# Kernel optimization log

Hardware: AMD Instinct MI355X
Metric: run time of the kernel (lower is better)

The kernel has to match this reference:

```python
import jax, jax.numpy as jnp
import numpy as np

N = 65536          # query points (rays * samples per chunk)
C = 2048           # num_codes in code cloud
K = 16             # knn neighbors
CD = 64            # code_dim
IN_XYZ = 63        # positional-encoded xyz channels
IN_DIR = 27        # positional-encoded dir channels
W = 128            # decoder width (D=4, skips=[2])
DIST_SCALE = 2.0


def setup_inputs() -> dict:
    key = jax.random.key(0)
    ks = jax.random.split(key, 16)

    def glorot(k, shape):
        return jax.random.normal(k, shape, jnp.float32) / np.float32(np.sqrt(shape[0]))

    in_x = CD + IN_XYZ  # decoder in_channels_xyz = 127
    inp = {
        "indices": jnp.zeros((1,), jnp.int32),
        "query_points": jax.random.uniform(ks[0], (N, 3), jnp.float32),
        "xyzdir_embedded": jax.random.normal(ks[1], (N, IN_XYZ + IN_DIR), jnp.float32),
        "codes_position": jax.random.uniform(ks[2], (1, C, 3), jnp.float32),
        "codes": jax.random.normal(ks[3], (1, C, CD), jnp.float32) * 0.01,
        # decoder params
        "W0": glorot(ks[4], (in_x, W)), "b0": jnp.zeros((W,), jnp.float32),
        "W1": glorot(ks[5], (W, W)), "b1": jnp.zeros((W,), jnp.float32),
        "W2": glorot(ks[6], (W + in_x, W)), "b2": jnp.zeros((W,), jnp.float32),  # skip layer i=2
        "W3": glorot(ks[7], (W, W)), "b3": jnp.zeros((W,), jnp.float32),
        "Wf": glorot(ks[8], (W, W)), "bf": jnp.zeros((W,), jnp.float32),          # xyz_encoding_final
        "Wd": glorot(ks[9], (W + IN_DIR, W // 2)), "bd": jnp.zeros((W // 2,), jnp.float32),
        "Ws": glorot(ks[10], (W, 1)), "bs": jnp.zeros((1,), jnp.float32),
        "Wr": glorot(ks[11], (W // 2, 3)), "br": jnp.zeros((3,), jnp.float32),
    }
    return inp


def _knn_idx(q, c, k):
    # brute-force L2 knn (faiss replacement); indices only, no grad (torch no_grad)
    q = jax.lax.stop_gradient(q)
    c = jax.lax.stop_gradient(c)
    d2 = (jnp.sum(q * q, -1, keepdims=True)
          - 2.0 * q @ c.T
          + jnp.sum(c * c, -1))  # (N, C)
    _, idx = jax.lax.top_k(-d2, k)  # (N, K) nearest
    return idx


def reference(indices, query_points, xyzdir_embedded, codes_position, codes,
              W0, b0, W1, b1, W2, b2, W3, b3, Wf, bf, Wd, bd, Ws, bs, Wr, br):
    # --- CodeCloud.query ---
    cp = codes_position[indices][0]      # (C, 3)
    cc = codes[indices][0]               # (C, CD)
    idx = _knn_idx(query_points, cp, K)  # (N, K)
    neigh_pos = cp[idx]                  # (N, K, 3)
    sq = jnp.sum((query_points[:, None, :] - neigh_pos) ** 2, -1) + 1e-16  # (N, K)
    w = 1.0 / jnp.sqrt(sq) ** DIST_SCALE
    w = w / jnp.sum(w, -1, keepdims=True)
    neigh_codes = cc[idx]                # (N, K, CD)
    query_codes = jnp.einsum("nk,nkd->nd", w, neigh_codes)  # (N, CD)

    # --- IM_Decoder (D=4, W=128, skips=[2]) ---
    x = jnp.concatenate([query_codes, xyzdir_embedded], -1)  # (N, 127+27)
    in_x = CD + IN_XYZ
    input_xyz, input_dir = x[:, :in_x], x[:, in_x:]
    h = jax.nn.relu(input_xyz @ W0 + b0)
    h = jax.nn.relu(h @ W1 + b1)
    h = jax.nn.relu(jnp.concatenate([input_xyz, h], -1) @ W2 + b2)  # skip at i=2
    h = jax.nn.relu(h @ W3 + b3)
    sigma = h @ Ws + bs                       # (N, 1)
    final = h @ Wf + bf                       # (N, W)
    d = jax.nn.relu(jnp.concatenate([final, input_dir], -1) @ Wd + bd)
    rgb = d @ Wr + br                         # (N, 3)
    return jnp.concatenate([rgb, sigma], -1)  # (N, 4)
```

## Files before the change

kernel.cpp:

```cpp
#include <hip/hip_runtime.h>

#define N_Q   65536
#define N_C   2048
#define KNN_K 16
#define CDIM  64
#define SLCAP 128
#define KINF  0x7FFFFFFF
#define WSZ   108544

typedef _Float16 half_t;
typedef float v4f __attribute__((ext_vector_type(4)));
typedef half_t v8h __attribute__((ext_vector_type(8)));

#define ASTRIDE 136
#define DSTRIDE 40

__device__ __forceinline__ int dppx(int v, int j){
  if (j == 1) return __builtin_amdgcn_mov_dpp(v, 0xB1,  0xF, 0xF, true);
  if (j == 2) return __builtin_amdgcn_mov_dpp(v, 0x4E,  0xF, 0xF, true);
  if (j == 8) return __builtin_amdgcn_mov_dpp(v, 0x128, 0xF, 0xF, true);
  return __shfl_xor(v, j, 64);
}
__device__ __forceinline__ float dppxf(float v, int j){
  return __int_as_float(dppx(__float_as_int(v), j));
}

__device__ __forceinline__ int select16th(int x){
  int P = 0;
#pragma unroll
  for (int b = 30; b >= 0; --b){
    int cand = P | (1 << b);
    unsigned long long m = __ballot(x < cand);
    if ((int)__popcll(m) < 16) P = cand;
  }
  return P;
}

__global__ void wtrans_kernel(const float* W0, const float* W1, const float* W2,
                              const float* W3, const float* Wf, const float* Wd,
                              const int* indices, const float* cpos,
                              half_t* wt, float4* cpos4){
  int idx = blockIdx.x * 256 + threadIdx.x;
  if (idx >= 110592) return;
  if (idx >= WSZ){
    int i = idx - WSZ;
    const float* cp = cpos + (size_t)indices[0] * N_C * 3;
    float x = cp[i*3 + 0], y = cp[i*3 + 1], z = cp[i*3 + 2];
    cpos4[i] = make_float4(x, y, z, fmaf(x, x, fmaf(y, y, fmaf(z, z, 4.0f))));
    return;
  }
  int base, nt, mode;
  const float* src = W1;
  if (idx < 16384){ base = 0; nt = 8; mode = 1; }
  else if (idx < 32768){ base = 16384; nt = 8; mode = 0; src = W1; }
  else if (idx < 65536){ base = 32768; nt = 8; mode = 2; }
  else if (idx < 81920){ base = 65536; nt = 8; mode = 0; src = W3; }
  else if (idx < 98304){ base = 81920; nt = 8; mode = 0; src = Wf; }
  else { base = 98304; nt = 4; mode = 3; }
  int i = idx - base;
  int tile = i >> 9, e = i & 511;
  int lane = e >> 3, j = e & 7;
  int k0idx = tile / nt, tcol = tile - k0idx*nt;
  int n = tcol*16 + (lane & 15);
  int k = k0idx*32 + ((lane >> 4) << 3) + j;
  float val;
  if (mode == 0)      val = src[k*128 + n];
  else if (mode == 1) val = (k < 127) ? W0[k*128 + n] : 0.f;
  else if (mode == 2) val = (k == 127) ? 0.f
                           : ((k < 127) ? W2[k*128 + n] : W2[(k-1)*128 + n]);
  else                val = (k < 155) ? Wd[k*64 + n] : 0.f;
  wt[idx] = (half_t)val;
}

__global__ __launch_bounds__(512, 6) void knn_kernel(const int* indices,
    const float* qpts, const float4* cpos4, const float* codes,
    const float* xyzdir, half_t* Ain, half_t* Din){
  __shared__ float4 lp[N_C];
  __shared__ int    sl[8*SLCAP];
  int tid = threadIdx.x;
  int lane = tid & 63, wave = tid >> 6;
  const float* cc = codes + (size_t)indices[0] * N_C * CDIM;

  for (int c = tid; c < N_C; c += 512) lp[c] = cpos4[c];
  __syncthreads();

  int q = blockIdx.x * 8 + wave;
  float qx = qpts[q*3 + 0];
  float qy = qpts[q*3 + 1];
  float qz = qpts[q*3 + 2];
  float nqx = -2.0f*qx, nqy = -2.0f*qy, nqz = -2.0f*qz;

  int p[32];
#pragma unroll
  for (int j = 0; j < 32; j++){
    int c = j*64 + lane;
    float4 P = lp[c];
    float s = fmaf(P.x, nqx, fmaf(P.y, nqy, fmaf(P.z, nqz, P.w)));
    int pv = (__float_as_int(s) & 0xFFFFF800) | c;
    asm("" : "+v"(pv));
    p[j] = pv;
  }

  int lm = p[0];
#pragma unroll
  for (int j = 1; j < 32; j++) lm = min(lm, p[j]);

  int tau = select16th(lm);

  int* slw = &sl[wave * SLCAP];
  int n = 0;
#pragma unroll
  for (int j = 0; j < 32; j++){
    bool c = (p[j] <= tau);
    unsigned long long m = __ballot(c);
    if (m){
      if (n <= 64){
        if (c){
          int mb = __builtin_amdgcn_mbcnt_hi((unsigned)(m >> 32),
                   __builtin_amdgcn_mbcnt_lo((unsigned)m, 0));
          slw[n + mb] = p[j];
        }
      }
      n += (int)__popcll(m);
    }
  }
  __builtin_amdgcn_wave_barrier();

  int keep;
  if (n >= KNN_K && n <= 64){
    int x = (lane < n) ? slw[lane] : KINF;
    int P2 = select16th(x);
    unsigned long long wmask = __ballot(x <= P2);
    int pos = __builtin_amdgcn_mbcnt_hi((unsigned)(wmask >> 32),
              __builtin_amdgcn_mbcnt_lo((unsigned)wmask, 0));
    if (x <= P2) slw[pos] = x;
    __builtin_amdgcn_wave_barrier();
    keep = (lane < KNN_K) ? slw[lane] : KINF;
  } else {
    keep = KINF;
#pragma unroll 1
    for (int rr = 0; rr < KNN_K; rr++){
      int lmf = p[0];
#pragma unroll
      for (int j = 1; j < 32; j++) lmf = min(lmf, p[j]);
      int gm = lmf;
#pragma unroll
      for (int off2 = 1; off2 < 64; off2 <<= 1)
        gm = min(gm, __shfl_xor(gm, off2, 64));
      if (lane == rr) keep = gm;
#pragma unroll
      for (int j = 0; j < 32; j++) p[j] = (p[j] == gm) ? KINF : p[j];
    }
  }

  int ci = keep & 0x7FF;
  float4 P = lp[ci];
  float dx = qx - P.x, dy = qy - P.y, dz = qz - P.z;
  float d2 = fmaf(dz, dz, fmaf(dy, dy, dx*dx));
  float w = 1.0f / (d2 + 1e-16f);
  float wm = (lane < KNN_K) ? w : 0.0f;
  wm += dppxf(wm, 1);
  wm += dppxf(wm, 2);
  wm += __shfl_xor(wm, 4, 64);
  wm += dppxf(wm, 8);
  float wn = w / wm;

  float acc = 0.f;
#pragma unroll
  for (int i = 0; i < KNN_K; i++){
    int   cb = __shfl(ci, i, 64);
    float wb = __shfl(wn, i, 64);
    acc = fmaf(wb, cc[cb*CDIM + lane], acc);
  }
  size_t arow = (size_t)q * ASTRIDE;
  Ain[arow + lane] = (half_t)acc;

  float xv = (lane < 63) ? xyzdir[(size_t)q*90 + lane] : 0.f;
  Ain[arow + 64 + lane] = (half_t)xv;
  if (lane < 8) Ain[arow + 128 + lane] = (half_t)0.f;
  if (lane < 40){
    float dv = (lane < 27) ? xyzdir[(size_t)q*90 + 63 + lane] : 0.f;
    Din[(size_t)q*DSTRIDE + lane] = (half_t)dv;
  }
}

template<int NCH, int NT>
__device__ inline void mfma_pl(const half_t* act, int astride, int rowbase,
                               const half_t* wlayer, int nt, int ktbase,
                               int tcolbase, v4f acc[2][NT], int lane){
  v8h breg[NCH*NT];
#pragma unroll
  for (int c = 0; c < NCH; c++){
#pragma unroll
    for (int t = 0; t < NT; t++){
      const half_t* bp = wlayer +
          ((size_t)(((ktbase + c)*nt + tcolbase + t) << 9) + (lane << 3));
      breg[c*NT + t] = *(const v8h*)bp;
    }
  }
  int m = lane & 15, quad = lane >> 4;
#pragma unroll
  for (int c = 0; c < NCH; c++){
    v8h a0 = *(const v8h*)&act[(rowbase + m)*astride + c*32 + quad*8];
    v8h a1 = *(const v8h*)&act[(rowbase + 16 + m)*astride + c*32 + quad*8];
#pragma unroll
    for (int t = 0; t < NT; t++){
      acc[0][t] = __builtin_amdgcn_mfma_f32_16x16x32_f16(a0, breg[c*NT + t], acc[0][t], 0, 0, 0);
      acc[1][t] = __builtin_amdgcn_mfma_f32_16x16x32_f16(a1, breg[c*NT + t], acc[1][t], 0, 0, 0);
    }
  }
}

template<int NT>
__device__ inline void epilogue64(v4f acc[2][NT], half_t* outb, int rowbase,
                                  int colbase, const float* bias, bool relu,
                                  int lane){
  int n = lane & 15, quad = lane >> 4;
#pragma unroll
  for (int t = 0; t < NT; t++){
    int col = colbase + t*16 + n;
    float bv = bias[col];
#pragma unroll
    for (int g = 0; g < 2; g++){
#pragma unroll
      for (int r = 0; r < 4; r++){
        float v = acc[g][t][r] + bv;
        if (relu) v = fmaxf(v, 0.f);
        outb[(rowbase + g*16 + quad*4 + r)*ASTRIDE + col] = (half_t)v;
      }
    }
  }
}

__global__ __launch_bounds__(512, 6) void mlp_mfma(
    const half_t* Ain, const half_t* Din, const half_t* wt,
    const float* b0, const float* b1, const float* b2, const float* b3,
    const float* bfb, const float* bdb,
    const float* Wsb, const float* bsb, const float* Wrb, const float* brb,
    float* out){
  __shared__ __align__(16) half_t Abuf[64*ASTRIDE];
  __shared__ __align__(16) half_t Pbuf[64*ASTRIDE];
  __shared__ __align__(16) half_t Qbuf[64*ASTRIDE];

  int tid = threadIdx.x, lane = tid & 63, wave = tid >> 6;
  int qbase = blockIdx.x * 64;

  for (int i = tid; i < 64*17; i += 512){
    int r = i / 17, c8 = i - r*17;
    *(uint4*)&Abuf[r*ASTRIDE + (c8 << 3)] =
        *(const uint4*)&Ain[(size_t)(qbase + r)*ASTRIDE + (c8 << 3)];
  }
  __syncthreads();

  int rowbase  = (wave >> 2) * 32;
  int colq     = wave & 3;
  int colbase  = colq * 32;
  int tcolbase = colq * 2;
  v4f acc[2][2];
  v4f accd[2][1];

  const half_t* wt0 = wt;
  const half_t* wt1 = wt + 16384;
  const half_t* wt2 = wt + 32768;
  const half_t* wt3 = wt + 65536;
  const half_t* wtf = wt + 81920;
  const half_t* wtd = wt + 98304;

#define ZACC22() { for (int g_ = 0; g_ < 2; g_++) for (int t_ = 0; t_ < 2; t_++) \
                   for (int e_ = 0; e_ < 4; e_++) acc[g_][t_][e_] = 0.f; }

  ZACC22();
  mfma_pl<4,2>(Abuf, ASTRIDE, rowbase, wt0, 8, 0, tcolbase, acc, lane);
  epilogue64<2>(acc, Pbuf, rowbase, colbase, b0, true, lane);
  __syncthreads();

  ZACC22();
  mfma_pl<4,2>(Pbuf, ASTRIDE, rowbase, wt1, 8, 0, tcolbase, acc, lane);
  epilogue64<2>(acc, Qbuf, rowbase, colbase, b1, true, lane);
  __syncthreads();

  ZACC22();
  mfma_pl<4,2>(Abuf, ASTRIDE, rowbase, wt2, 8, 0, tcolbase, acc, lane);
  mfma_pl<4,2>(Qbuf, ASTRIDE, rowbase, wt2, 8, 4, tcolbase, acc, lane);
  epilogue64<2>(acc, Pbuf, rowbase, colbase, b2, true, lane);
  __syncthreads();

  ZACC22();
  mfma_pl<4,2>(Pbuf, ASTRIDE, rowbase, wt3, 8, 0, tcolbase, acc, lane);
  epilogue64<2>(acc, Abuf, rowbase, colbase, b3, true, lane);
  __syncthreads();

  ZACC22();
  mfma_pl<4,2>(Abuf, ASTRIDE, rowbase, wtf, 8, 0, tcolbase, acc, lane);
  epilogue64<2>(acc, Pbuf, rowbase, colbase, bfb, false, lane);
  __syncthreads();

#pragma unroll
  for (int g_ = 0; g_ < 2; g_++)
#pragma unroll
    for (int e_ = 0; e_ < 4; e_++) accd[g_][0][e_] = 0.f;
  mfma_pl<4,1>(Pbuf, ASTRIDE, rowbase, wtd, 4, 0, colq, accd, lane);
  mfma_pl<1,1>(Din + (size_t)qbase*DSTRIDE, DSTRIDE, rowbase, wtd, 4, 4, colq,
               accd, lane);
  epilogue64<1>(accd, Qbuf, rowbase, colq * 16, bdb, true, lane);
  __syncthreads();

  {
    int q = tid >> 3, part = tid & 7;
    float s = 0.f;
#pragma unroll
    for (int k = 0; k < 16; k++){
      int kk = part*16 + k;
      s = fmaf((float)Abuf[q*ASTRIDE + kk], Wsb[kk], s);
    }
    s += __shfl_xor(s, 1, 64); s += __shfl_xor(s, 2, 64); s += __shfl_xor(s, 4, 64);

    float r3[3];
#pragma unroll
    for (int c2 = 0; c2 < 3; c2++){
      float rv = 0.f;
#pragma unroll
      for (int k = 0; k < 8; k++){
        int kk = part*8 + k;
        rv = fmaf((float)Qbuf[q*ASTRIDE + kk], Wrb[kk*3 + c2], rv);
      }
      rv += __shfl_xor(rv, 1, 64); rv += __shfl_xor(rv, 2, 64); rv += __shfl_xor(rv, 4, 64);
      r3[c2] = rv;
    }
    if (part == 0){
      size_t ob = ((size_t)(qbase + q)) * 4;
      out[ob + 0] = r3[0] + brb[0];
      out[ob + 1] = r3[1] + brb[1];
      out[ob + 2] = r3[2] + brb[2];
      out[ob + 3] = s + bsb[0];
    }
  }
}

extern "C" void kernel_launch(void* const* d_in, const int* in_sizes, int n_in,
                              void* d_out, int out_size, void* d_ws, size_t ws_size,
                              hipStream_t stream){
  (void)in_sizes; (void)n_in; (void)out_size; (void)ws_size;

  const int*   indices = (const int*)d_in[0];
  const float* qpts    = (const float*)d_in[1];
  const float* xyzdir  = (const float*)d_in[2];
  const float* cpos    = (const float*)d_in[3];
  const float* codes   = (const float*)d_in[4];
  const float* W0 = (const float*)d_in[5];
  const float* b0 = (const float*)d_in[6];
  const float* W1 = (const float*)d_in[7];
  const float* b1 = (const float*)d_in[8];
  const float* W2 = (const float*)d_in[9];
  const float* b2 = (const float*)d_in[10];
  const float* W3 = (const float*)d_in[11];
  const float* b3 = (const float*)d_in[12];
  const float* Wf = (const float*)d_in[13];
  const float* bf = (const float*)d_in[14];
  const float* Wd = (const float*)d_in[15];
  const float* bd = (const float*)d_in[16];
  const float* Ws = (const float*)d_in[17];
  const float* bs = (const float*)d_in[18];
  const float* Wr = (const float*)d_in[19];
  const float* br = (const float*)d_in[20];

  half_t* Ain   = (half_t*)d_ws;
  half_t* Din   = (half_t*)((char*)d_ws + 17825792);
  half_t* wt    = (half_t*)((char*)d_ws + 17825792 + 5242880);
  float4* cpos4 = (float4*)((char*)d_ws + 17825792 + 5242880 + 217088);

  wtrans_kernel<<<(110592 + 255)/256, 256, 0, stream>>>(W0, W1, W2, W3, Wf, Wd,
                                                        indices, cpos, wt, cpos4);
  knn_kernel<<<N_Q/8, 512, 0, stream>>>(indices, qpts, cpos4, codes, xyzdir,
                                        Ain, Din);
  mlp_mfma<<<N_Q/64, 512, 0, stream>>>(Ain, Din, wt,
                                       b0, b1, b2, b3, bf, bd, Ws, bs, Wr, br,
                                       (float*)d_out);
}
```

Before: 203.2 us.

## Use uniform grid candidate lists to prune brute-force KNN search

Adds a grid kernel that bins the 2048 code positions into a 16^3 grid and, for each cell, records candidates lying in a 7^3 neighbourhood. The KNN kernel then scores at most 256 candidates per query instead of all 2048. It checks whether the 16th distance lies within the distance to the neighbourhood boundary and otherwise falls back to an exact streaming brute-force selection. The radix select is also narrowed to fewer bits because the biased distance is known to be at least 4.0. This cuts distance evaluations and register pressure, at the cost of an extra kernel launch, a list lookup and a possible slow fallback path.

```diff
diff --git a/kernel.cpp b/kernel.cpp
--- a/kernel.cpp
+++ b/kernel.cpp
@@ -8,6 +8,10 @@
 #define KINF  0x7FFFFFFF
 #define WSZ   108544
 
+#define GN     16
+#define GCELLS 4096
+#define LCAP   256
+
 typedef _Float16 half_t;
 typedef float v4f __attribute__((ext_vector_type(4)));
 typedef half_t v8h __attribute__((ext_vector_type(8)));
@@ -25,15 +29,42 @@
   return __int_as_float(dppx(__float_as_int(v), j));
 }
 
-__device__ __forceinline__ int select16th(int x){
-  int P = 0;
-#pragma unroll
-  for (int b = 30; b >= 0; --b){
+__device__ __forceinline__ int select16f(int x){
+  int P = 0x40800000;
+#pragma unroll
+  for (int b = 22; b >= 0; --b){
     int cand = P | (1 << b);
     unsigned long long m = __ballot(x < cand);
     if ((int)__popcll(m) < 16) P = cand;
   }
   return P;
+}
+
+__device__ __forceinline__ int knn_fallback(const float4* lp, float nqx,
+                                            float nqy, float nqz, int lane){
+  unsigned used = 0u;
+  int keep = KINF;
+#pragma unroll 1
+  for (int rr = 0; rr < KNN_K; rr++){
+    int best = KINF;
+#pragma unroll 1
+    for (int j = 0; j < 32; j++){
+      int c = j*64 + lane;
+      float4 P = lp[c];
+      float s = fmaf(P.x, nqx, fmaf(P.y, nqy, fmaf(P.z, nqz, P.w)));
+      int pv = (__float_as_int(s) & 0xFFFFF800) | c;
+      pv = ((used >> j) & 1u) ? KINF : pv;
+      best = min(best, pv);
+    }
+    int gm = best;
+#pragma unroll
+    for (int off2 = 1; off2 < 64; off2 <<= 1)
+      gm = min(gm, __shfl_xor(gm, off2, 64));
+    if (lane == rr) keep = gm;
+    int gc = gm & 0x7FF;
+    if ((gc & 63) == lane) used |= (1u << (gc >> 6));
+  }
+  return keep;
 }
 
 __global__ void wtrans_kernel(const float* W0, const float* W1, const float* W2,
@@ -72,9 +103,40 @@
   wt[idx] = (half_t)val;
 }
 
+__global__ __launch_bounds__(512) void grid_kernel(const float4* cpos4,
+    unsigned short* list, int* cnt){
+  int lane = threadIdx.x & 63, wave = threadIdx.x >> 6;
+  int c = blockIdx.x * 8 + wave;
+  int cx = c & 15, cy = (c >> 4) & 15, cz = c >> 8;
+  int lox = min(max(cx - 3, 0), 9);
+  int loy = min(max(cy - 3, 0), 9);
+  int loz = min(max(cz - 3, 0), 9);
+  unsigned short* L = list + (size_t)c * LCAP;
+  int n = 0;
+#pragma unroll 1
+  for (int b = 0; b < 32; b++){
+    int i = b * 64 + lane;
+    float4 P = cpos4[i];
+    int ix = min((int)(P.x * 16.0f), 15);
+    int iy = min((int)(P.y * 16.0f), 15);
+    int iz = min((int)(P.z * 16.0f), 15);
+    bool in = ((unsigned)(ix - lox) < 7u) && ((unsigned)(iy - loy) < 7u) &&
+              ((unsigned)(iz - loz) < 7u);
+    unsigned long long m = __ballot(in);
+    if (m){
+      int mb = __builtin_amdgcn_mbcnt_hi((unsigned)(m >> 32),
+               __builtin_amdgcn_mbcnt_lo((unsigned)m, 0));
+      if (in && (n + mb) < LCAP) L[n + mb] = (unsigned short)i;
+      n += (int)__popcll(m);
+    }
+  }
+  if (lane == 0) cnt[c] = (n <= LCAP) ? n : 0;
+}
+
 __global__ __launch_bounds__(512, 6) void knn_kernel(const int* indices,
-    const float* qpts, const float4* cpos4, const float* codes,
-    const float* xyzdir, half_t* Ain, half_t* Din){
+    const float* qpts, const float4* cpos4, const unsigned short* list,
+    const int* cnt, const float* codes, const float* xyzdir,
+    half_t* Ain, half_t* Din){
   __shared__ float4 lp[N_C];
   __shared__ int    sl[8*SLCAP];
   int tid = threadIdx.x;
@@ -90,35 +152,45 @@
   float qz = qpts[q*3 + 2];
   float nqx = -2.0f*qx, nqy = -2.0f*qy, nqz = -2.0f*qz;
 
-  int p[32];
-#pragma unroll
-  for (int j = 0; j < 32; j++){
-    int c = j*64 + lane;
-    float4 P = lp[c];
+  int cx = min((int)(qx * 16.0f), 15);
+  int cy = min((int)(qy * 16.0f), 15);
+  int cz = min((int)(qz * 16.0f), 15);
+  int cell = cx | (cy << 4) | (cz << 8);
+  int lox = min(max(cx - 3, 0), 9);
+  int loy = min(max(cy - 3, 0), 9);
+  int loz = min(max(cz - 3, 0), 9);
+  int nl = cnt[cell];
+  const unsigned short* L = list + (size_t)cell * LCAP;
+
+  int p[4];
+  int lanemin = KINF;
+#pragma unroll
+  for (int it = 0; it < 4; it++){
+    int j = it*64 + lane;
+    int idx = L[j] & 2047;
+    float4 P = lp[idx];
     float s = fmaf(P.x, nqx, fmaf(P.y, nqy, fmaf(P.z, nqz, P.w)));
-    int pv = (__float_as_int(s) & 0xFFFFF800) | c;
+    int pv = (__float_as_int(s) & 0xFFFFF800) | idx;
+    pv = (j < nl) ? pv : KINF;
     asm("" : "+v"(pv));
-    p[j] = pv;
-  }
-
-  int lm = p[0];
-#pragma unroll
-  for (int j = 1; j < 32; j++) lm = min(lm, p[j]);
-
-  int tau = select16th(lm);
+    p[it] = pv;
+    lanemin = min(lanemin, pv);
+  }
+
+  int tau = select16f(lanemin);
 
   int* slw = &sl[wave * SLCAP];
   int n = 0;
 #pragma unroll
-  for (int j = 0; j < 32; j++){
-    bool c = (p[j] <= tau);
+  for (int it = 0; it < 4; it++){
+    bool c = (p[it] <= tau);
     unsigned long long m = __ballot(c);
     if (m){
       if (n <= 64){
         if (c){
           int mb = __builtin_amdgcn_mbcnt_hi((unsigned)(m >> 32),
                    __builtin_amdgcn_mbcnt_lo((unsigned)m, 0));
-          slw[n + mb] = p[j];
+          slw[n + mb] = p[it];
         }
       }
       n += (int)__popcll(m);
@@ -126,32 +198,30 @@
   }
   __builtin_amdgcn_wave_barrier();
 
-  int keep;
+  int keep = KINF;
+  bool need_fb = true;
   if (n >= KNN_K && n <= 64){
     int x = (lane < n) ? slw[lane] : KINF;
-    int P2 = select16th(x);
+    int P2 = select16f(x);
     unsigned long long wmask = __ballot(x <= P2);
     int pos = __builtin_amdgcn_mbcnt_hi((unsigned)(wmask >> 32),
               __builtin_amdgcn_mbcnt_lo((unsigned)wmask, 0));
     if (x <= P2) slw[pos] = x;
     __builtin_amdgcn_wave_barrier();
     keep = (lane < KNN_K) ? slw[lane] : KINF;
-  } else {
-    keep = KINF;
-#pragma unroll 1
-    for (int rr = 0; rr < KNN_K; rr++){
-      int lmf = p[0];
-#pragma unroll
-      for (int j = 1; j < 32; j++) lmf = min(lmf, p[j]);
-      int gm = lmf;
-#pragma unroll
-      for (int off2 = 1; off2 < 64; off2 <<= 1)
-        gm = min(gm, __shfl_xor(gm, off2, 64));
-      if (lane == rr) keep = gm;
-#pragma unroll
-      for (int j = 0; j < 32; j++) p[j] = (p[j] == gm) ? KINF : p[j];
-    }
-  }
+
+    float d2u = __int_as_float(P2 & 0xFFFFF800) - 4.0f + 0.001f;
+    float lofx = lox * 0.0625f, lofy = loy * 0.0625f, lofz = loz * 0.0625f;
+    float cl = 1e9f;
+    if (lox > 0) cl = fminf(cl, qx - lofx);
+    if (lox < 9) cl = fminf(cl, lofx + 0.4375f - qx);
+    if (loy > 0) cl = fminf(cl, qy - lofy);
+    if (loy < 9) cl = fminf(cl, lofy + 0.4375f - qy);
+    if (loz > 0) cl = fminf(cl, qz - lofz);
+    if (loz < 9) cl = fminf(cl, lofz + 0.4375f - qz);
+    need_fb = !(d2u <= cl * cl);
+  }
+  if (need_fb) keep = knn_fallback(lp, nqx, nqy, nqz, lane);
 
   int ci = keep & 0x7FF;
   float4 P = lp[ci];
@@ -364,15 +434,18 @@
   const float* Wr = (const float*)d_in[19];
   const float* br = (const float*)d_in[20];
 
-  half_t* Ain   = (half_t*)d_ws;
-  half_t* Din   = (half_t*)((char*)d_ws + 17825792);
-  half_t* wt    = (half_t*)((char*)d_ws + 17825792 + 5242880);
-  float4* cpos4 = (float4*)((char*)d_ws + 17825792 + 5242880 + 217088);
+  half_t* Ain            = (half_t*)d_ws;
+  half_t* Din            = (half_t*)((char*)d_ws + 17825792);
+  half_t* wt             = (half_t*)((char*)d_ws + 23068672);
+  float4* cpos4          = (float4*)((char*)d_ws + 23285760);
+  unsigned short* list   = (unsigned short*)((char*)d_ws + 23318528);
+  int* cnt               = (int*)((char*)d_ws + 25415680);
 
   wtrans_kernel<<<(110592 + 255)/256, 256, 0, stream>>>(W0, W1, W2, W3, Wf, Wd,
                                                         indices, cpos, wt, cpos4);
-  knn_kernel<<<N_Q/8, 512, 0, stream>>>(indices, qpts, cpos4, codes, xyzdir,
-                                        Ain, Din);
+  grid_kernel<<<GCELLS/8, 512, 0, stream>>>(cpos4, list, cnt);
+  knn_kernel<<<N_Q/8, 512, 0, stream>>>(indices, qpts, cpos4, list, cnt,
+                                        codes, xyzdir, Ain, Din);
   mlp_mfma<<<N_Q/64, 512, 0, stream>>>(Ain, Din, wt,
                                        b0, b1, b2, b3, bf, bd, Ws, bs, Wr, br,
                                        (float*)d_out);
```

Result: slower. 705.4 us (+247.1%).
